# Optimization experiments

Hardware: AMD Instinct MI355X
Metric: run time of the kernel (lower is better)

The kernel has to match this reference:

```python
import jax, jax.numpy as jnp
import numpy as np

DIM = 1024


def setup_inputs() -> dict:
    key = jax.random.key(0)
    ks = jax.random.split(key, 12)
    d = DIM
    B, T = 8, 4096
    s = 1.0 / np.sqrt(d)
    return {
        "x": jax.random.normal(ks[0], (B, T, d), dtype=jnp.float32),
        "u": jnp.ones((d,), dtype=jnp.float32),
        "w": jnp.ones((d,), dtype=jnp.float32),
        "tmk": jnp.ones((d,), dtype=jnp.float32),
        "tmv": jnp.ones((d,), dtype=jnp.float32),
        "tmr": jnp.ones((d,), dtype=jnp.float32),
        "Wk": jax.random.normal(ks[1], (d, d), dtype=jnp.float32) * s,
        "Wv": jax.random.normal(ks[2], (d, d), dtype=jnp.float32) * s,
        "Wr": jax.random.normal(ks[3], (d, d), dtype=jnp.float32) * s,
        "Wo": jax.random.normal(ks[4], (d, d), dtype=jnp.float32) * s,
        "bo": jnp.zeros((d,), dtype=jnp.float32),
    }


def _wkv_scan(k, v, u, w):
    # k, v: [B, T, d]; u, w: [d]
    kT = jnp.swapaxes(k, 0, 1)  # [T, B, d]
    vT = jnp.swapaxes(v, 0, 1)

    def step(carry, kv_t):
        a, b = carry
        k_t, v_t = kv_t
        q = jnp.maximum(u + k_t, w)
        e1 = jnp.exp(-w - q)
        e2 = jnp.exp(u + k_t - q)
        a = e1 * a + e2 * v_t
        b = e1 * b + e2
        return (a, b), a / b

    B, _, d = k.shape
    init = (jnp.zeros((B, d), k.dtype), jnp.zeros((B, d), k.dtype))
    _, wkvT = jax.lax.scan(step, init, (kT, vT))
    return jnp.swapaxes(wkvT, 0, 1)  # [B, T, d]


def reference(x, u, w, tmk, tmv, tmr, Wk, Wv, Wr, Wo, bo):
    # time_shift: zero-pad one step at front, drop last -> x_shifted[t] = x[t-1]
    x_sh = jnp.pad(x, ((0, 0), (1, 0), (0, 0)))[:, :-1, :]
    key = x * tmk + x_sh * (1.0 - tmk)
    value = x * tmv + x_sh * (1.0 - tmv)
    receptance = jax.nn.sigmoid(x * tmr + x_sh * (1.0 - tmr))
    # torch Linear(no bias): y = x @ W.T
    k = jnp.einsum("btd,ed->bte", key, Wk)
    v = jnp.einsum("btd,ed->bte", value, Wv)
    r = jnp.einsum("btd,ed->bte", receptance, Wr)
    wkv = _wkv_scan(k, v, u, w)
    return jnp.einsum("btd,ed->bte", wkv * r, Wo) + bo
```

## Files before the change

kernel.cpp:

```cpp
#include <hip/hip_runtime.h>

#define DIMD 1024
#define BATCH 8
#define SEQ 4096
#define TCH 32
#define NCH (SEQ / TCH)

typedef short short8 __attribute__((ext_vector_type(8)));
typedef unsigned short u16x8 __attribute__((ext_vector_type(8)));
typedef __bf16 bf16x8 __attribute__((ext_vector_type(8)));
typedef float f32x4 __attribute__((ext_vector_type(4)));

static __device__ __forceinline__ unsigned short f2bf(float f) {
    unsigned int u = __builtin_bit_cast(unsigned int, f);
    u += 0x7FFFu + ((u >> 16) & 1u);
    return (unsigned short)(u >> 16);
}
static __device__ __forceinline__ float bf2f(unsigned short s) {
    return __builtin_bit_cast(float, ((unsigned int)s) << 16);
}

__global__ void detect(const unsigned* __restrict__ xw, unsigned* __restrict__ flag) {
    if (threadIdx.x == 0 && blockIdx.x == 0) {
        int cnt = 0;
        for (int i = 0; i < 64; ++i) {
            unsigned lo = xw[i] & 0xFFFFu;
            unsigned e = (lo >> 7) & 0xFFu;
            if ((e >= 0x70u && e <= 0x8Fu) || lo == 0u) ++cnt;
        }
        *flag = (cnt >= 32) ? 1u : 0u;
    }
}

__global__ void cvt_small(const void* __restrict__ s0, const void* __restrict__ s1,
                          const void* __restrict__ s2, const void* __restrict__ s3,
                          const void* __restrict__ s4, const void* __restrict__ s5,
                          float* __restrict__ dst, const unsigned* __restrict__ flag) {
    const void* s;
    switch (blockIdx.y) {
        case 0: s = s0; break; case 1: s = s1; break; case 2: s = s2; break;
        case 3: s = s3; break; case 4: s = s4; break; default: s = s5; break;
    }
    int i = blockIdx.x * 256 + threadIdx.x;
    float v = (*flag) ? bf2f(((const unsigned short*)s)[i]) : ((const float*)s)[i];
    dst[blockIdx.y * 1024 + i] = v;
}

__global__ void cvt_W(const void* __restrict__ s0, const void* __restrict__ s1,
                      const void* __restrict__ s2, const void* __restrict__ s3,
                      unsigned short* __restrict__ dst, const unsigned* __restrict__ flag) {
    const void* s;
    switch (blockIdx.y) {
        case 0: s = s0; break; case 1: s = s1; break;
        case 2: s = s2; break; default: s = s3; break;
    }
    unsigned short* d = dst + (size_t)blockIdx.y * DIMD * DIMD;
    size_t i8 = (size_t)blockIdx.x * 256 + threadIdx.x;
    if (*flag) {
        ((u16x8*)d)[i8] = ((const u16x8*)s)[i8];
    } else {
        const float4* s4 = (const float4*)s;
        float4 a = s4[i8 * 2], b = s4[i8 * 2 + 1];
        u16x8 o;
        o[0] = f2bf(a.x); o[1] = f2bf(a.y); o[2] = f2bf(a.z); o[3] = f2bf(a.w);
        o[4] = f2bf(b.x); o[5] = f2bf(b.y); o[6] = f2bf(b.z); o[7] = f2bf(b.w);
        ((u16x8*)d)[i8] = o;
    }
}

__global__ void prep3(const void* __restrict__ xb, size_t xoff,
                      const float* __restrict__ tmk, const float* __restrict__ tmv,
                      const float* __restrict__ tmr,
                      unsigned short* __restrict__ mix3, size_t mstride,
                      const unsigned* __restrict__ flag) {
    size_t i8 = (size_t)blockIdx.x * 256 + threadIdx.x;
    int d8 = (int)(i8 & 127);
    size_t row = i8 >> 7;
    int t = (int)(row & (SEQ - 1));
    float xv[8], xs[8];
    if (*flag) {
        const unsigned short* x = (const unsigned short*)xb + xoff;
        u16x8 a = ((const u16x8*)x)[i8];
#pragma unroll
        for (int j = 0; j < 8; ++j) xv[j] = bf2f(a[j]);
        if (t > 0) {
            u16x8 b = ((const u16x8*)x)[i8 - 128];
#pragma unroll
            for (int j = 0; j < 8; ++j) xs[j] = bf2f(b[j]);
        } else {
#pragma unroll
            for (int j = 0; j < 8; ++j) xs[j] = 0.f;
        }
    } else {
        const float* x = (const float*)xb + xoff;
        const float4* x4 = (const float4*)x;
        float4 a0 = x4[i8 * 2], a1 = x4[i8 * 2 + 1];
        xv[0]=a0.x; xv[1]=a0.y; xv[2]=a0.z; xv[3]=a0.w;
        xv[4]=a1.x; xv[5]=a1.y; xv[6]=a1.z; xv[7]=a1.w;
        if (t > 0) {
            float4 b0 = x4[i8 * 2 - 256], b1 = x4[i8 * 2 - 255];
            xs[0]=b0.x; xs[1]=b0.y; xs[2]=b0.z; xs[3]=b0.w;
            xs[4]=b1.x; xs[5]=b1.y; xs[6]=b1.z; xs[7]=b1.w;
        } else {
#pragma unroll
            for (int j = 0; j < 8; ++j) xs[j] = 0.f;
        }
    }
    const float4* k4 = (const float4*)tmk;
    const float4* v4 = (const float4*)tmv;
    const float4* r4 = (const float4*)tmr;
    float4 mk0 = k4[d8*2], mk1 = k4[d8*2+1];
    float4 mv0 = v4[d8*2], mv1 = v4[d8*2+1];
    float4 mr0 = r4[d8*2], mr1 = r4[d8*2+1];
    float mk[8] = {mk0.x,mk0.y,mk0.z,mk0.w, mk1.x,mk1.y,mk1.z,mk1.w};
    float mv[8] = {mv0.x,mv0.y,mv0.z,mv0.w, mv1.x,mv1.y,mv1.z,mv1.w};
    float mr[8] = {mr0.x,mr0.y,mr0.z,mr0.w, mr1.x,mr1.y,mr1.z,mr1.w};
    u16x8 ok, ov, orr;
#pragma unroll
    for (int j = 0; j < 8; ++j) {
        float dxy = xv[j] - xs[j];
        ok[j] = f2bf(xs[j] + mk[j] * dxy);
        ov[j] = f2bf(xs[j] + mv[j] * dxy);
        float r = xs[j] + mr[j] * dxy;
        orr[j] = f2bf(1.f / (1.f + __expf(-r)));
    }
    ((u16x8*)(mix3))[i8] = ok;
    ((u16x8*)(mix3 + mstride))[i8] = ov;
    ((u16x8*)(mix3 + 2 * mstride))[i8] = orr;
}


static __device__ __forceinline__ void stage_half(
    const unsigned short* __restrict__ g, unsigned short* l, int tid)
{
#pragma unroll
    for (int ld = 0; ld < 2; ++ld) {
        int c = ld * 512 + tid;
        int row = c >> 3;
        int jj = c & 7;
        int kA = (jj ^ (row & 7)) * 8;
        __builtin_amdgcn_global_load_lds(
            (const __attribute__((address_space(1))) void*)(g + (size_t)row * DIMD + kA),
            (__attribute__((address_space(3))) void*)(l + c * 8), 16, 0, 0);
    }
}

#define SA_L(buf, h) (lds + (buf) * 16384 + (h) * 8192)
#define SB_L(buf, h) (lds + 32768 + (buf) * 16384 + (h) * 8192)
#define STA(buf, h, t) stage_half(A + (row0 + (h) * 128) * DIMD + (t) * 64, SA_L(buf, h), tid)
#define STB(buf, h, t) stage_half(Wp + (col0 + (h) * 128) * DIMD + (t) * 64, SB_L(buf, h), tid)

#define PH(Q, BUF, STAGES, TAIL)                                                   \
    {                                                                              \
        const unsigned short* sAb = lds + (BUF) * 16384;                           \
        const unsigned short* sBb = lds + 32768 + (BUF) * 16384;                   \
        short8 af[2][2];                                                           \
        if ((Q) == 0) {                                                            \
            _Pragma("unroll") for (int nt = 0; nt < 4; ++nt)                       \
            _Pragma("unroll") for (int kh = 0; kh < 2; ++kh) {                     \
                int r = wn + nt * 16 + l15;                                        \
                int j = (kh * 4 + qd) ^ (r & 7);                                   \
                bfr[nt][kh] = *(const short8*)(sBb + r * 64 + j * 8);              \
            }                                                                      \
        }                                                                          \
        _Pragma("unroll") for (int m2 = 0; m2 < 2; ++m2)                           \
        _Pragma("unroll") for (int kh = 0; kh < 2; ++kh) {                         \
            int r = wm + ((Q) * 2 + m2) * 16 + l15;                                \
            int j = (kh * 4 + qd) ^ (r & 7);                                       \
            af[m2][kh] = *(const short8*)(sAb + r * 64 + j * 8);                   \
        }                                                                          \
        STAGES;                                                                    \
        asm volatile("s_barrier" ::: "memory");                                    \
        __builtin_amdgcn_s_setprio(1);                                             \
        _Pragma("unroll") for (int m2 = 0; m2 < 2; ++m2)                           \
        _Pragma("unroll") for (int nt = 0; nt < 4; ++nt)                           \
        _Pragma("unroll") for (int kh = 0; kh < 2; ++kh)                           \
            acc[(Q) * 2 + m2][nt] = __builtin_amdgcn_mfma_f32_16x16x32_bf16(       \
                __builtin_bit_cast(bf16x8, af[m2][kh]),                            \
                __builtin_bit_cast(bf16x8, bfr[nt][kh]),                           \
                acc[(Q) * 2 + m2][nt], 0, 0, 0);                                   \
        __builtin_amdgcn_s_setprio(0);                                             \
        TAIL;                                                                      \
        asm volatile("s_barrier" ::: "memory");                                    \
    }

__global__ __launch_bounds__(512, 2) void gemm_fused(
    const unsigned short* __restrict__ Aall,
    const unsigned short* __restrict__ Wall,
    const float* __restrict__ biasf,
    void* __restrict__ Cout, size_t coff,
    int M, int nx, int force_bf16, const unsigned* __restrict__ flag)
{
    __shared__ unsigned short lds[65536];

    const int tid = threadIdx.x;
    const int lane = tid & 63;
    const int wv = tid >> 6;
    const int wm = (wv >> 2) * 128;
    const int wn = (wv & 3) * 64;
    const int l15 = lane & 15;
    const int qd = lane >> 4;

    const int id = blockIdx.x;
    const int cls = id & 7;
    const int sub = id >> 3;
    const int bx = sub % nx;
    const int by = cls + 8 * (sub / nx);
    const int which = bx >> 2;
    const unsigned short* A  = Aall + (size_t)which * M * DIMD;
    const unsigned short* Wp = Wall + (size_t)which * DIMD * DIMD;
    const size_t row0 = (size_t)by * 256;
    const size_t col0 = (size_t)(bx & 3) * 256;

    f32x4 acc[8][4];
#pragma unroll
    for (int i = 0; i < 8; ++i)
#pragma unroll
        for (int j = 0; j < 4; ++j)
            acc[i][j] = {0.f, 0.f, 0.f, 0.f};

    short8 bfr[4][2];

    STB(0, 0, 0); STB(0, 1, 0);
    STA(0, 0, 0); STA(0, 1, 0);
    STB(1, 0, 1); STB(1, 1, 1);
    asm volatile("s_waitcnt vmcnt(4)" ::: "memory");
    asm volatile("s_barrier" ::: "memory");

    for (int it = 0; it < 8; ++it) {
        const int o  = 2 * it + 1;
        const int e2 = 2 * it + 2;
        const int o2 = 2 * it + 3;
        const bool pre = (it < 7);
        PH(0, 0, { STA(1, 0, o); }, {});
        PH(1, 0, { STA(1, 1, o); }, {});
        PH(2, 0, { if (pre) STB(0, 0, e2); }, {});
        PH(3, 0, { if (pre) STB(0, 1, e2); },
                 { if (pre) { asm volatile("s_waitcnt vmcnt(4)" ::: "memory"); }
                   else     { asm volatile("s_waitcnt vmcnt(0)" ::: "memory"); } });
        PH(0, 1, { if (pre) STA(0, 0, e2); }, {});
        PH(1, 1, { if (pre) STA(0, 1, e2); }, {});
        PH(2, 1, { if (pre) STB(1, 0, o2); }, {});
        PH(3, 1, { if (pre) STB(1, 1, o2); },
                 { if (pre) { asm volatile("s_waitcnt vmcnt(4)" ::: "memory"); } });
    }

    const bool wb16 = force_bf16 || (*flag != 0u);
    const size_t cbase = coff + (size_t)which * M * DIMD;
    if (wb16) {
        unsigned short* sC = lds;
        float bvv[4];
#pragma unroll
        for (int nt = 0; nt < 4; ++nt)
            bvv[nt] = biasf ? biasf[col0 + wn + nt * 16 + l15] : 0.f;
#pragma unroll
        for (int mt = 0; mt < 8; ++mt)
#pragma unroll
        for (int nt = 0; nt < 4; ++nt)
#pragma unroll
        for (int i = 0; i < 4; ++i) {
            int row = wm + mt * 16 + qd * 4 + i;
            int col = wn + nt * 16 + l15;
            int j = col >> 3;
            int js = j ^ (((row >> 2) & 3) << 1);
            sC[row * 256 + js * 8 + (col & 7)] = f2bf(acc[mt][nt][i] + bvv[nt]);
        }
        __syncthreads();
        unsigned short* Cb = (unsigned short*)Cout;
#pragma unroll
        for (int ch = 0; ch < 16; ++ch) {
            int c = ch * 512 + tid;
            int row = c >> 5;
            int jj = c & 31;
            int js = jj ^ (((row >> 2) & 3) << 1);
            short8 vv = *(const short8*)(sC + row * 256 + js * 8);
            *(u16x8*)(Cb + cbase + (row0 + row) * DIMD + col0 + jj * 8) =
                __builtin_bit_cast(u16x8, vv);
        }
    } else {
        float* Cf = (float*)Cout;
#pragma unroll
        for (int nt = 0; nt < 4; ++nt) {
            size_t gc = col0 + wn + nt * 16 + l15;
            float bv = biasf ? biasf[gc] : 0.f;
#pragma unroll
            for (int mt = 0; mt < 8; ++mt)
#pragma unroll
            for (int i = 0; i < 4; ++i) {
                size_t gr = row0 + wm + mt * 16 + qd * 4 + i;
                Cf[cbase + gr * DIMD + gc] = acc[mt][nt][i] + bv;
            }
        }
    }
}

__global__ void wkv_pass1(const unsigned short* __restrict__ kk,
                          const unsigned short* __restrict__ vv,
                          const float* __restrict__ uf, const float* __restrict__ wf,
                          float* __restrict__ aloc, float* __restrict__ bloc,
                          float* __restrict__ pp, int nchan)
{
    const int e0 = (threadIdx.x & 127) * 8;
    const int c  = blockIdx.z * 2 + (threadIdx.x >> 7);
    const int b  = blockIdx.y;
    float u8[8], w8[8];
    *(float4*)(u8)     = *(const float4*)(uf + e0);
    *(float4*)(u8 + 4) = *(const float4*)(uf + e0 + 4);
    *(float4*)(w8)     = *(const float4*)(wf + e0);
    *(float4*)(w8 + 4) = *(const float4*)(wf + e0 + 4);

    size_t base = ((size_t)(b * SEQ + c * TCH)) * DIMD + e0;
    float a[8], bb[8], P[8];
#pragma unroll
    for (int j = 0; j < 8; ++j) { a[j] = 0.f; bb[j] = 0.f; P[j] = 1.f; }

    for (int t = 0; t < TCH; ++t) {
        u16x8 k8 = *(const u16x8*)(kk + base + (size_t)t * DIMD);
        u16x8 v8 = *(const u16x8*)(vv + base + (size_t)t * DIMD);
#pragma unroll
        for (int j = 0; j < 8; ++j) {
            float kt = bf2f(k8[j]);
            float vt = bf2f(v8[j]);
            float q = fmaxf(u8[j] + kt, w8[j]);
            float e1 = __expf(fminf(-w8[j] - q, 60.f));
            float e2 = __expf(u8[j] + kt - q);
            a[j] = e1 * a[j] + e2 * vt;
            bb[j] = e1 * bb[j] + e2;
            P[j] *= e1;
        }
    }
    size_t si = (size_t)c * nchan + b * DIMD + e0;
#pragma unroll
    for (int j = 0; j < 8; ++j) P[j] = fminf(fmaxf(P[j], 0.f), 1e30f);
    *(float4*)(aloc + si)     = *(const float4*)(a);
    *(float4*)(aloc + si + 4) = *(const float4*)(a + 4);
    *(float4*)(bloc + si)     = *(const float4*)(bb);
    *(float4*)(bloc + si + 4) = *(const float4*)(bb + 4);
    *(float4*)(pp + si)       = *(const float4*)(P);
    *(float4*)(pp + si + 4)   = *(const float4*)(P + 4);
}

__global__ void wkv_pass2(const float* __restrict__ aloc, const float* __restrict__ bloc,
                          const float* __restrict__ pp,
                          float* __restrict__ ain, float* __restrict__ bin, int nchan)
{
    int ch = blockIdx.x * 256 + threadIdx.x;
    float a = 0.f, b = 0.f;
    for (int c = 0; c < NCH; ++c) {
        size_t si = (size_t)c * nchan + ch;
        ain[si] = a; bin[si] = b;
        float P = pp[si];
        a = fmaf(P, a, aloc[si]);
        b = fmaf(P, b, bloc[si]);
    }
}

__global__ void wkv_pass3(const unsigned short* __restrict__ kk,
                          const unsigned short* __restrict__ vv,
                          const unsigned short* __restrict__ rr,
                          const float* __restrict__ uf, const float* __restrict__ wf,
                          const float* __restrict__ ain, const float* __restrict__ bin,
                          unsigned short* __restrict__ ao, int nchan)
{
    const int e0 = (threadIdx.x & 127) * 8;
    const int c  = blockIdx.z * 2 + (threadIdx.x >> 7);
    const int b  = blockIdx.y;
    float u8[8], w8[8];
    *(float4*)(u8)     = *(const float4*)(uf + e0);
    *(float4*)(u8 + 4) = *(const float4*)(uf + e0 + 4);
    *(float4*)(w8)     = *(const float4*)(wf + e0);
    *(float4*)(w8 + 4) = *(const float4*)(wf + e0 + 4);

    size_t base = ((size_t)(b * SEQ + c * TCH)) * DIMD + e0;
    size_t si = (size_t)c * nchan + b * DIMD + e0;
    float a[8], bb[8];
    *(float4*)(a)      = *(const float4*)(ain + si);
    *(float4*)(a + 4)  = *(const float4*)(ain + si + 4);
    *(float4*)(bb)     = *(const float4*)(bin + si);
    *(float4*)(bb + 4) = *(const float4*)(bin + si + 4);

    for (int t = 0; t < TCH; ++t) {
        size_t gi = base + (size_t)t * DIMD;
        u16x8 k8 = *(const u16x8*)(kk + gi);
        u16x8 v8 = *(const u16x8*)(vv + gi);
        u16x8 r8 = *(const u16x8*)(rr + gi);
        u16x8 o8;
#pragma unroll
        for (int j = 0; j < 8; ++j) {
            float kt = bf2f(k8[j]);
            float vt = bf2f(v8[j]);
            float q = fmaxf(u8[j] + kt, w8[j]);
            float e1 = __expf(fminf(-w8[j] - q, 60.f));
            float e2 = __expf(u8[j] + kt - q);
            a[j] = e1 * a[j] + e2 * vt;
            bb[j] = e1 * bb[j] + e2;
            float wkv = a[j] / fmaxf(bb[j], 1e-38f);
            o8[j] = f2bf(wkv * bf2f(r8[j]));
        }
        *(u16x8*)(ao + gi) = o8;
    }
}

extern "C" void kernel_launch(void* const* d_in, const int* in_sizes, int n_in,
                              void* d_out, int out_size, void* d_ws, size_t ws_size,
                              hipStream_t stream) {
    const void* x   = d_in[0];
    const void* u   = d_in[1];
    const void* w   = d_in[2];
    const void* tmk = d_in[3];
    const void* tmv = d_in[4];
    const void* tmr = d_in[5];
    const void* Wk  = d_in[6];
    const void* Wv  = d_in[7];
    const void* Wr  = d_in[8];
    const void* Wo  = d_in[9];
    const void* bo  = d_in[10];
    (void)in_sizes; (void)n_in; (void)out_size;

    const size_t MB = 1ull << 20;
    int nb;
    if      (ws_size >= 432 * MB) nb = 8;
    else if (ws_size >= 124 * MB) nb = 2;
    else                          nb = 1;
    const int ngroups = BATCH / nb;
    const size_t Mg = (size_t)nb * SEQ;
    const int nchan = nb * DIMD;

    char* ws = (char*)d_ws;
    unsigned* flag = (unsigned*)(ws);
    float* smallf  = (float*)(ws + 64 * 1024);
    unsigned short* Wb = (unsigned short*)(ws + 1 * MB);
    unsigned short* mix3 = (unsigned short*)(ws + 16 * MB);
    size_t matB = Mg * DIMD * sizeof(unsigned short);
    unsigned short* kvr = (unsigned short*)((char*)mix3 + 3 * matB);
    char* sc = (char*)kvr + 3 * matB;
    size_t scanB = (size_t)NCH * nchan * sizeof(float);
    float* aloc = (float*)(sc + 0 * scanB);
    float* bloc = (float*)(sc + 1 * scanB);
    float* pp   = (float*)(sc + 2 * scanB);
    float* ain  = (float*)(sc + 3 * scanB);
    float* bin  = (float*)(sc + 4 * scanB);

    float* uf   = smallf + 0 * 1024;
    float* wf   = smallf + 1 * 1024;
    float* tmkf = smallf + 2 * 1024;
    float* tmvf = smallf + 3 * 1024;
    float* tmrf = smallf + 4 * 1024;
    float* bof  = smallf + 5 * 1024;
    unsigned short* Wob = Wb + 3ull * DIMD * DIMD;

    detect<<<1, 64, 0, stream>>>((const unsigned*)x, flag);
    cvt_small<<<dim3(4, 6), 256, 0, stream>>>(u, w, tmk, tmv, tmr, bo, smallf, flag);
    cvt_W<<<dim3(512, 4), 256, 0, stream>>>(Wk, Wv, Wr, Wo, Wb, flag);

    const size_t mstride = Mg * DIMD;
    unsigned short* kk  = kvr;
    unsigned short* vvb = kvr + mstride;
    unsigned short* rrb = kvr + 2 * mstride;
    const int ny = (int)(Mg / 256);
    dim3 gScan(1, nb, NCH / 2);

    for (int g = 0; g < ngroups; ++g) {
        size_t xoff = (size_t)g * Mg * DIMD;

        prep3<<<(int)(Mg * DIMD / 8 / 256), 256, 0, stream>>>(
            x, xoff, tmkf, tmvf, tmrf, mix3, mstride, flag);
        gemm_fused<<<12 * ny, 512, 0, stream>>>(
            mix3, Wb, nullptr, kvr, 0, (int)Mg, 12, 1, flag);

        wkv_pass1<<<gScan, 256, 0, stream>>>(kk, vvb, uf, wf, aloc, bloc, pp, nchan);
        wkv_pass2<<<nchan / 256, 256, 0, stream>>>(aloc, bloc, pp, ain, bin, nchan);
        wkv_pass3<<<gScan, 256, 0, stream>>>(kk, vvb, rrb, uf, wf, ain, bin, kk, nchan);

        gemm_fused<<<4 * ny, 512, 0, stream>>>(
            kk, Wob, bof, d_out, xoff, (int)Mg, 4, 0, flag);
    }
}
```

Baseline: 669.1 us.

## Drop WKV carry-propagation pass and recompute chunk prefixes inside pass3

After: 754.8 us. 12.8% more time.

```diff
diff --git a/kernel.cpp b/kernel.cpp
--- a/kernel.cpp
+++ b/kernel.cpp
@@ -3,7 +3,7 @@
 #define DIMD 1024
 #define BATCH 8
 #define SEQ 4096
-#define TCH 32
+#define TCH 16
 #define NCH (SEQ / TCH)
 
 typedef short short8 __attribute__((ext_vector_type(8)));
@@ -32,39 +32,43 @@
     }
 }
 
-__global__ void cvt_small(const void* __restrict__ s0, const void* __restrict__ s1,
-                          const void* __restrict__ s2, const void* __restrict__ s3,
-                          const void* __restrict__ s4, const void* __restrict__ s5,
-                          float* __restrict__ dst, const unsigned* __restrict__ flag) {
-    const void* s;
-    switch (blockIdx.y) {
-        case 0: s = s0; break; case 1: s = s1; break; case 2: s = s2; break;
-        case 3: s = s3; break; case 4: s = s4; break; default: s = s5; break;
-    }
-    int i = blockIdx.x * 256 + threadIdx.x;
-    float v = (*flag) ? bf2f(((const unsigned short*)s)[i]) : ((const float*)s)[i];
-    dst[blockIdx.y * 1024 + i] = v;
-}
-
-__global__ void cvt_W(const void* __restrict__ s0, const void* __restrict__ s1,
-                      const void* __restrict__ s2, const void* __restrict__ s3,
-                      unsigned short* __restrict__ dst, const unsigned* __restrict__ flag) {
-    const void* s;
-    switch (blockIdx.y) {
-        case 0: s = s0; break; case 1: s = s1; break;
-        case 2: s = s2; break; default: s = s3; break;
-    }
-    unsigned short* d = dst + (size_t)blockIdx.y * DIMD * DIMD;
-    size_t i8 = (size_t)blockIdx.x * 256 + threadIdx.x;
-    if (*flag) {
-        ((u16x8*)d)[i8] = ((const u16x8*)s)[i8];
+__global__ void cvt_all(const void* __restrict__ w0, const void* __restrict__ w1,
+                        const void* __restrict__ w2, const void* __restrict__ w3,
+                        const void* __restrict__ v0, const void* __restrict__ v1,
+                        const void* __restrict__ v2, const void* __restrict__ v3,
+                        const void* __restrict__ v4, const void* __restrict__ v5,
+                        unsigned short* __restrict__ Wdst, float* __restrict__ sdst,
+                        const unsigned* __restrict__ flag) {
+    if (blockIdx.y < 4) {
+        const void* s;
+        switch (blockIdx.y) {
+            case 0: s = w0; break; case 1: s = w1; break;
+            case 2: s = w2; break; default: s = w3; break;
+        }
+        unsigned short* d = Wdst + (size_t)blockIdx.y * DIMD * DIMD;
+        size_t i8 = (size_t)blockIdx.x * 256 + threadIdx.x;
+        if (*flag) {
+            ((u16x8*)d)[i8] = ((const u16x8*)s)[i8];
+        } else {
+            const float4* s4 = (const float4*)s;
+            float4 a = s4[i8 * 2], b = s4[i8 * 2 + 1];
+            u16x8 o;
+            o[0] = f2bf(a.x); o[1] = f2bf(a.y); o[2] = f2bf(a.z); o[3] = f2bf(a.w);
+            o[4] = f2bf(b.x); o[5] = f2bf(b.y); o[6] = f2bf(b.z); o[7] = f2bf(b.w);
+            ((u16x8*)d)[i8] = o;
+        }
     } else {
-        const float4* s4 = (const float4*)s;
-        float4 a = s4[i8 * 2], b = s4[i8 * 2 + 1];
-        u16x8 o;
-        o[0] = f2bf(a.x); o[1] = f2bf(a.y); o[2] = f2bf(a.z); o[3] = f2bf(a.w);
-        o[4] = f2bf(b.x); o[5] = f2bf(b.y); o[6] = f2bf(b.z); o[7] = f2bf(b.w);
-        ((u16x8*)d)[i8] = o;
+        int idx = blockIdx.x * 256 + threadIdx.x;
+        if (idx < 6 * 1024) {
+            int vec = idx >> 10, i = idx & 1023;
+            const void* s;
+            switch (vec) {
+                case 0: s = v0; break; case 1: s = v1; break; case 2: s = v2; break;
+                case 3: s = v3; break; case 4: s = v4; break; default: s = v5; break;
+            }
+            float v = (*flag) ? bf2f(((const unsigned short*)s)[i]) : ((const float*)s)[i];
+            sdst[vec * 1024 + i] = v;
+        }
     }
 }
 
@@ -340,26 +344,12 @@
     *(float4*)(pp + si + 4)   = *(const float4*)(P + 4);
 }
 
-__global__ void wkv_pass2(const float* __restrict__ aloc, const float* __restrict__ bloc,
-                          const float* __restrict__ pp,
-                          float* __restrict__ ain, float* __restrict__ bin, int nchan)
-{
-    int ch = blockIdx.x * 256 + threadIdx.x;
-    float a = 0.f, b = 0.f;
-    for (int c = 0; c < NCH; ++c) {
-        size_t si = (size_t)c * nchan + ch;
-        ain[si] = a; bin[si] = b;
-        float P = pp[si];
-        a = fmaf(P, a, aloc[si]);
-        b = fmaf(P, b, bloc[si]);
-    }
-}
-
 __global__ void wkv_pass3(const unsigned short* __restrict__ kk,
                           const unsigned short* __restrict__ vv,
                           const unsigned short* __restrict__ rr,
                           const float* __restrict__ uf, const float* __restrict__ wf,
-                          const float* __restrict__ ain, const float* __restrict__ bin,
+                          const float* __restrict__ aloc, const float* __restrict__ bloc,
+                          const float* __restrict__ pp,
                           unsigned short* __restrict__ ao, int nchan)
 {
     const int e0 = (threadIdx.x & 127) * 8;
@@ -371,14 +361,28 @@
     *(float4*)(w8)     = *(const float4*)(wf + e0);
     *(float4*)(w8 + 4) = *(const float4*)(wf + e0 + 4);
 
+    float a[8], bb[8];
+#pragma unroll
+    for (int j = 0; j < 8; ++j) { a[j] = 0.f; bb[j] = 0.f; }
+    size_t sbase = (size_t)b * DIMD + e0;
+#pragma unroll 4
+    for (int cc = 0; cc < c; ++cc) {
+        size_t si = (size_t)cc * nchan + sbase;
+        float P8[8], al[8], bl[8];
+        *(float4*)(P8)     = *(const float4*)(pp + si);
+        *(float4*)(P8 + 4) = *(const float4*)(pp + si + 4);
+        *(float4*)(al)     = *(const float4*)(aloc + si);
+        *(float4*)(al + 4) = *(const float4*)(aloc + si + 4);
+        *(float4*)(bl)     = *(const float4*)(bloc + si);
+        *(float4*)(bl + 4) = *(const float4*)(bloc + si + 4);
+#pragma unroll
+        for (int j = 0; j < 8; ++j) {
+            a[j]  = fmaf(P8[j], a[j], al[j]);
+            bb[j] = fmaf(P8[j], bb[j], bl[j]);
+        }
+    }
+
     size_t base = ((size_t)(b * SEQ + c * TCH)) * DIMD + e0;
-    size_t si = (size_t)c * nchan + b * DIMD + e0;
-    float a[8], bb[8];
-    *(float4*)(a)      = *(const float4*)(ain + si);
-    *(float4*)(a + 4)  = *(const float4*)(ain + si + 4);
-    *(float4*)(bb)     = *(const float4*)(bin + si);
-    *(float4*)(bb + 4) = *(const float4*)(bin + si + 4);
-
     for (int t = 0; t < TCH; ++t) {
         size_t gi = base + (size_t)t * DIMD;
         u16x8 k8 = *(const u16x8*)(kk + gi);
@@ -419,8 +423,8 @@
 
     const size_t MB = 1ull << 20;
     int nb;
-    if      (ws_size >= 432 * MB) nb = 8;
-    else if (ws_size >= 124 * MB) nb = 2;
+    if      (ws_size >= 430 * MB) nb = 8;
+    else if (ws_size >= 122 * MB) nb = 2;
     else                          nb = 1;
     const int ngroups = BATCH / nb;
     const size_t Mg = (size_t)nb * SEQ;
@@ -438,8 +442,6 @@
     float* aloc = (float*)(sc + 0 * scanB);
     float* bloc = (float*)(sc + 1 * scanB);
     float* pp   = (float*)(sc + 2 * scanB);
-    float* ain  = (float*)(sc + 3 * scanB);
-    float* bin  = (float*)(sc + 4 * scanB);
 
     float* uf   = smallf + 0 * 1024;
     float* wf   = smallf + 1 * 1024;
@@ -450,8 +452,9 @@
     unsigned short* Wob = Wb + 3ull * DIMD * DIMD;
 
     detect<<<1, 64, 0, stream>>>((const unsigned*)x, flag);
-    cvt_small<<<dim3(4, 6), 256, 0, stream>>>(u, w, tmk, tmv, tmr, bo, smallf, flag);
-    cvt_W<<<dim3(512, 4), 256, 0, stream>>>(Wk, Wv, Wr, Wo, Wb, flag);
+    cvt_all<<<dim3(512, 5), 256, 0, stream>>>(Wk, Wv, Wr, Wo,
+                                              u, w, tmk, tmv, tmr, bo,
+                                              Wb, smallf, flag);
 
     const size_t mstride = Mg * DIMD;
     unsigned short* kk  = kvr;
@@ -469,10 +472,10 @@
             mix3, Wb, nullptr, kvr, 0, (int)Mg, 12, 1, flag);
 
         wkv_pass1<<<gScan, 256, 0, stream>>>(kk, vvb, uf, wf, aloc, bloc, pp, nchan);
-        wkv_pass2<<<nchan / 256, 256, 0, stream>>>(aloc, bloc, pp, ain, bin, nchan);
-        wkv_pass3<<<gScan, 256, 0, stream>>>(kk, vvb, rrb, uf, wf, ain, bin, kk, nchan);
-
-        gemm_fused<<<4 * ny, 512, 0, stream>>>(
+        wkv_pass3<<<gScan, 256, 0, stream>>>(kk, vvb, rrb, uf, wf,
+                                             aloc, bloc, pp, kk, nchan);
+
+        gemm_fused<<<8 * ny / 2, 512, 0, stream>>>(
             kk, Wob, bof, d_out, xoff, (int)Mg, 4, 0, flag);
     }
 }
```
